# Optimization experiments

Hardware: AMD Instinct MI355X
Metric: run time of the kernel (lower is better)

Reference implementation:

```python
import jax, jax.numpy as jnp
import numpy as np

NUM_EMBEDDINGS = 1024
EMBEDDING_DIM = 256


def setup_inputs() -> dict:
    key = jax.random.key(0)
    k1, k2 = jax.random.split(key)
    input = jax.random.normal(k1, (64, 32, 32, EMBEDDING_DIM), dtype=jnp.float32)
    weight = jax.random.normal(k2, (NUM_EMBEDDINGS, EMBEDDING_DIM), dtype=jnp.float32)
    return {"input": input, "weight": weight}


def reference(input, weight):
    # Nearest-code lookup: argmin_k 0.5*||mu_k||^2 - <z, mu_k>  (scaled by 2 here,
    # matching torch: sqr - 2*cov). weight: [K, D], input: [..., D].
    sqr = jnp.sum(weight * weight, axis=1)                      # [K]
    cov = jnp.einsum('...j,kj->...k', input, weight)            # [..., K]
    indices = jnp.argmin(sqr - 2.0 * cov, axis=-1)              # [...]
    vectors = jnp.take(weight, indices, axis=0)                 # [..., D]
    # Straight-through estimator: values == vectors, grad flows to input.
    values = jax.lax.stop_gradient(vectors - input) + input
    return values, indices, vectors
```

## Files before the change

### kernel.cpp

```cpp
#include <hip/hip_runtime.h>


constexpr int N_TOK = 65536;
constexpr int KC    = 1024;
constexpr int D     = 256;

constexpr size_t IDX_OFF = (size_t)N_TOK * D;
constexpr size_t VEC_OFF = IDX_OFF + N_TOK;
constexpr int    WL_CAP  = 16777216;

#define MARGIN 12.0f

typedef __attribute__((ext_vector_type(8))) short bf16x8;
typedef __attribute__((ext_vector_type(4))) float f32x4;

__device__ inline unsigned short f2bf(float x) {
    unsigned int u = __float_as_uint(x);
    unsigned int r = (u + 0x7FFFu + ((u >> 16) & 1u)) >> 16;
    return (unsigned short)r;
}

__device__ inline unsigned int fkey(float f) {
    unsigned int b = __float_as_uint(f);
    return (b & 0x80000000u) ? ~b : (b | 0x80000000u);
}

__global__ __launch_bounds__(64)
void vq_prep(const float* __restrict__ w, unsigned short* __restrict__ wbf,
             float* __restrict__ sqr, int* __restrict__ cnt) {
    const int code = blockIdx.x;
    const int lane = threadIdx.x;
    float4 v = ((const float4*)w)[(size_t)code * 64 + lane];
    float s = v.x * v.x + v.y * v.y + v.z * v.z + v.w * v.w;
#pragma unroll
    for (int off = 32; off >= 1; off >>= 1) s += __shfl_xor(s, off, 64);
    unsigned short* d = wbf + (size_t)code * D + lane * 4;
    d[0] = f2bf(v.x); d[1] = f2bf(v.y); d[2] = f2bf(v.z); d[3] = f2bf(v.w);
    if (lane == 0) sqr[code] = s;
    if (code == 0 && lane == 0) *cnt = 0;
}

constexpr int CT   = 32;
constexpr int NS   = KC / CT;
constexpr int LCAP = 3072;

struct __align__(16) P1Shared {
    unsigned short sbuf[2][CT * D];
    float sqr[KC];
    int   list[LCAP];
    int   lcnt, gbase;
};

__device__ __forceinline__ void stage32(const unsigned short* __restrict__ wbf,
                                        unsigned short* dstbuf, int s, int tid) {
#pragma unroll
    for (int r = 0; r < 4; ++r) {
        const int dchunk = tid + r * 256;
        const int cc     = dchunk >> 5;
        const int ch     = dchunk & 31;
        const unsigned short* src =
            wbf + (((size_t)(s * CT + cc)) << 8) + ((ch ^ (cc & 7)) << 3);
        unsigned short* dst = dstbuf + (dchunk << 3);
        __builtin_amdgcn_global_load_lds(
            (const __attribute__((address_space(1))) void*)src,
            (__attribute__((address_space(3))) void*)dst, 16, 0, 0);
    }
}

template<bool EMIT>
__device__ __forceinline__ void scan(const unsigned short* __restrict__ wbf,
                                     P1Shared& sh,
                                     const bf16x8 (&a)[2][8],
                                     float (&rmin)[2][4],
                                     int row_base, int tid, int lane, int col, int quad,
                                     int* __restrict__ wl, int* __restrict__ cnt) {
    stage32(wbf, sh.sbuf[0], 0, tid);
    __syncthreads();
    for (int s = 0; s < NS; ++s) {
        if (s + 1 < NS) stage32(wbf, sh.sbuf[(s + 1) & 1], s + 1, tid);
        const unsigned short* sb = sh.sbuf[s & 1];
#pragma unroll
        for (int tt = 0; tt < 2; ++tt) {
            const int ccl = tt * 16 + col;
            const int c0  = s * CT + tt * 16;
            bf16x8 b[8];
#pragma unroll
            for (int kt = 0; kt < 8; ++kt) {
                const int ch = (quad + 4 * kt) ^ (ccl & 7);
                b[kt] = *(const bf16x8*)(sb + ccl * 256 + ch * 8);
            }
            const float sq = sh.sqr[c0 + col];
#pragma unroll
            for (int rt = 0; rt < 2; ++rt) {
                f32x4 acc = {0.f, 0.f, 0.f, 0.f};
#pragma unroll
                for (int kt = 0; kt < 8; ++kt)
                    acc = __builtin_amdgcn_mfma_f32_16x16x32_bf16(a[rt][kt], b[kt], acc, 0, 0, 0);
                if (!EMIT) {
#pragma unroll
                    for (int rg = 0; rg < 4; ++rg)
                        rmin[rt][rg] = fminf(rmin[rt][rg], sq - 2.0f * acc[rg]);
                } else {
#pragma unroll
                    for (int rg = 0; rg < 4; ++rg) {
                        const float sc = sq - 2.0f * acc[rg];
                        const bool flag = (sc <= rmin[rt][rg] + MARGIN);
                        unsigned long long mask = __ballot(flag);
                        if (mask) {
                            const int leader = __builtin_ctzll(mask);
                            const int nact   = __popcll(mask);
                            const int prefix = __popcll(mask & ((1ULL << lane) - 1ULL));
                            int wbase = 0;
                            if (lane == leader) wbase = atomicAdd(&sh.lcnt, nact);
                            wbase = __shfl(wbase, leader, 64);
                            if (flag) {
                                const int row  = row_base + rt * 16 + quad * 4 + rg;
                                const int item = (row << 10) | (c0 + col);
                                const int pos  = wbase + prefix;
                                if (pos < LCAP) {
                                    sh.list[pos] = item;
                                } else {
                                    int g = atomicAdd(cnt, 1);
                                    if (g < WL_CAP) wl[g] = item;
                                }
                            }
                        }
                    }
                }
            }
        }
        __syncthreads();
    }
}

__global__ __launch_bounds__(256)
void vq_pass1(const float* __restrict__ input, const unsigned short* __restrict__ wbf,
              const float* __restrict__ sqr, int* __restrict__ wl,
              int* __restrict__ cnt, unsigned long long* __restrict__ cand) {
    __shared__ P1Shared sh;

    const int tid  = threadIdx.x;
    const int wave = tid >> 6;
    const int lane = tid & 63;
    const int col  = lane & 15;
    const int quad = lane >> 4;
    const int row_base = blockIdx.x * 128 + wave * 32;

    if (tid == 0) sh.lcnt = 0;
    ((float4*)sh.sqr)[tid] = ((const float4*)sqr)[tid];
    if (lane < 32) cand[row_base + lane] = 0xFFFFFFFFFFFFFFFFULL;

    bf16x8 a[2][8];
#pragma unroll
    for (int rt = 0; rt < 2; ++rt) {
        const float* ar = input + (size_t)(row_base + rt * 16 + col) * D;
#pragma unroll
        for (int kt = 0; kt < 8; ++kt) {
            const int k0 = kt * 32 + quad * 8;
            float4 f0 = *(const float4*)(ar + k0);
            float4 f1 = *(const float4*)(ar + k0 + 4);
            bf16x8 v;
            v[0] = (short)f2bf(f0.x); v[1] = (short)f2bf(f0.y);
            v[2] = (short)f2bf(f0.z); v[3] = (short)f2bf(f0.w);
            v[4] = (short)f2bf(f1.x); v[5] = (short)f2bf(f1.y);
            v[6] = (short)f2bf(f1.z); v[7] = (short)f2bf(f1.w);
            a[rt][kt] = v;
        }
    }

    float rmin[2][4];
#pragma unroll
    for (int rt = 0; rt < 2; ++rt)
#pragma unroll
        for (int rg = 0; rg < 4; ++rg) rmin[rt][rg] = 3.4e38f;

    scan<false>(wbf, sh, a, rmin, row_base, tid, lane, col, quad, wl, cnt);

#pragma unroll
    for (int off = 1; off <= 8; off <<= 1)
#pragma unroll
        for (int rt = 0; rt < 2; ++rt)
#pragma unroll
            for (int rg = 0; rg < 4; ++rg)
                rmin[rt][rg] = fminf(rmin[rt][rg], __shfl_xor(rmin[rt][rg], off, 64));

    scan<true>(wbf, sh, a, rmin, row_base, tid, lane, col, quad, wl, cnt);

    __syncthreads();
    const int n = min(sh.lcnt, LCAP);
    if (tid == 0) sh.gbase = atomicAdd(cnt, n);
    __syncthreads();
    const int base = sh.gbase;
    for (int i = tid; i < n; i += 256) wl[base + i] = sh.list[i];
}

__global__ __launch_bounds__(256)
void vq_pass2(const float* __restrict__ input, const float* __restrict__ weight,
              const float* __restrict__ sqr, const int* __restrict__ wl,
              const int* __restrict__ cnt, unsigned long long* __restrict__ cand) {
    const int sw  = threadIdx.x >> 4;
    const int sl  = threadIdx.x & 15;
    const int gsw = blockIdx.x * 16 + sw;
    const int nsw = gridDim.x * 16;
    const int n   = min(*cnt, WL_CAP);
    const float4* in4 = (const float4*)input;
    const float4* w4  = (const float4*)weight;

    for (int e = gsw; e < n; e += nsw) {
        const int ent  = wl[e];
        const int row  = ent >> 10;
        const int code = ent & 1023;
        const float4* zr = in4 + (size_t)row * 64;
        const float4* wr = w4 + (size_t)code * 64;
        float s = 0.f;
#pragma unroll
        for (int j = 0; j < 4; ++j) {
            float4 za = zr[sl + 16 * j];
            float4 wa = wr[sl + 16 * j];
            s = fmaf(za.x, wa.x, s);
            s = fmaf(za.y, wa.y, s);
            s = fmaf(za.z, wa.z, s);
            s = fmaf(za.w, wa.w, s);
        }
#pragma unroll
        for (int off = 1; off <= 8; off <<= 1) s += __shfl_xor(s, off, 16);
        if (sl == 0) {
            const float score = sqr[code] - 2.0f * s;
            unsigned long long key =
                ((unsigned long long)fkey(score) << 32) | (unsigned int)code;
            atomicMin(&cand[row], key);
        }
    }
}

__global__ __launch_bounds__(256)
void vq_pass3(const float* __restrict__ weight,
              const unsigned long long* __restrict__ cand,
              float* __restrict__ out) {
    __shared__ int fin[64];
    const int tid  = threadIdx.x;
    const int row0 = blockIdx.x * 64;
    if (tid < 64) {
        int idx = (int)(unsigned int)(cand[row0 + tid] & 0xFFFFFFFFULL);
        fin[tid] = idx;
        out[IDX_OFF + row0 + tid] = (float)idx;
    }
    __syncthreads();
    const float4* w4 = (const float4*)weight;
    float4* out4 = (float4*)out;
#pragma unroll
    for (int k = 0; k < 16; ++k) {
        int i = tid + k * 256;
        int r = i >> 6, q = i & 63;
        float4 v = w4[(size_t)fin[r] * 64 + q];
        size_t o = (size_t)(row0 + r) * 64 + q;
        out4[o] = v;
        out4[VEC_OFF / 4 + o] = v;
    }
}

extern "C" void kernel_launch(void* const* d_in, const int* in_sizes, int n_in,
                              void* d_out, int out_size, void* d_ws, size_t ws_size,
                              hipStream_t stream) {
    const float* input  = (const float*)d_in[0];
    const float* weight = (const float*)d_in[1];
    float* out = (float*)d_out;

    unsigned short* wbf = (unsigned short*)d_ws;
    float* sqr = (float*)((char*)d_ws + 524288);
    int*   cnt = (int*)((char*)d_ws + 528384);
    unsigned long long* cand = (unsigned long long*)((char*)d_ws + 532480);

    int* wl = (int*)out;

    vq_prep <<<KC, 64, 0, stream>>>(weight, wbf, sqr, cnt);
    vq_pass1<<<N_TOK / 128, 256, 0, stream>>>(input, wbf, sqr, wl, cnt, cand);
    vq_pass2<<<1024, 256, 0, stream>>>(input, weight, sqr, wl, cnt, cand);
    vq_pass3<<<N_TOK / 64, 256, 0, stream>>>(weight, cand, out);
}
```

Baseline: 306.3 us.

## Tile pass1 as 2x2 waves with triple-buffered codebook staging

Pass 1 now arranges its four waves in a 2x2 grid: each wave handles 64 rows and 16 codes per stage, instead of 32 rows over all 32 codes. This halves the LDS B-fragment reads per MFMA. Codebook staging moves to three buffers with two stages in flight, explicit vmcnt waits and a single barrier per stage. The staging source offsets are precomputed so that LDS reads become contiguous, and the per-row minima from the two column waves are merged through shared memory. The A-fragment registers double, and launch bounds ask for two blocks per CU, which adds register pressure and a larger LDS footprint.

```diff
diff --git a/kernel.cpp b/kernel.cpp
--- a/kernel.cpp
+++ b/kernel.cpp
@@ -41,99 +41,99 @@
 }
 
 constexpr int CT   = 32;
-constexpr int NS   = KC / CT;
+constexpr int NSTG = KC / CT;
 constexpr int LCAP = 3072;
 
 struct __align__(16) P1Shared {
-    unsigned short sbuf[2][CT * D];
+    unsigned short sbuf[3][CT * D];
     float sqr[KC];
+    float rminx[2][128];
     int   list[LCAP];
     int   lcnt, gbase;
 };
 
-__device__ __forceinline__ void stage32(const unsigned short* __restrict__ wbf,
-                                        unsigned short* dstbuf, int s, int tid) {
+__device__ __forceinline__ void stage_issue(const char* __restrict__ srcbase,
+                                            unsigned short* __restrict__ dstbuf,
+                                            const int (&soff)[4], int tid) {
 #pragma unroll
     for (int r = 0; r < 4; ++r) {
-        const int dchunk = tid + r * 256;
-        const int cc     = dchunk >> 5;
-        const int ch     = dchunk & 31;
-        const unsigned short* src =
-            wbf + (((size_t)(s * CT + cc)) << 8) + ((ch ^ (cc & 7)) << 3);
-        unsigned short* dst = dstbuf + (dchunk << 3);
         __builtin_amdgcn_global_load_lds(
-            (const __attribute__((address_space(1))) void*)src,
-            (__attribute__((address_space(3))) void*)dst, 16, 0, 0);
+            (const __attribute__((address_space(1))) void*)(srcbase + soff[r]),
+            (__attribute__((address_space(3))) void*)(dstbuf + (tid + r * 256) * 8),
+            16, 0, 0);
     }
 }
 
 template<bool EMIT>
-__device__ __forceinline__ void scan(const unsigned short* __restrict__ wbf,
-                                     P1Shared& sh,
-                                     const bf16x8 (&a)[2][8],
-                                     float (&rmin)[2][4],
-                                     int row_base, int tid, int lane, int col, int quad,
+__device__ __forceinline__ void scan(const char* __restrict__ wbfB, P1Shared& sh,
+                                     const bf16x8 (&a)[4][8], float (&rmin)[4][4],
+                                     int row_base_blk, int wr, int wc,
+                                     int tid, int lane, int col, int quad,
+                                     const int (&soff)[4],
                                      int* __restrict__ wl, int* __restrict__ cnt) {
-    stage32(wbf, sh.sbuf[0], 0, tid);
-    __syncthreads();
-    for (int s = 0; s < NS; ++s) {
-        if (s + 1 < NS) stage32(wbf, sh.sbuf[(s + 1) & 1], s + 1, tid);
-        const unsigned short* sb = sh.sbuf[s & 1];
-#pragma unroll
-        for (int tt = 0; tt < 2; ++tt) {
-            const int ccl = tt * 16 + col;
-            const int c0  = s * CT + tt * 16;
-            bf16x8 b[8];
-#pragma unroll
-            for (int kt = 0; kt < 8; ++kt) {
-                const int ch = (quad + 4 * kt) ^ (ccl & 7);
-                b[kt] = *(const bf16x8*)(sb + ccl * 256 + ch * 8);
-            }
-            const float sq = sh.sqr[c0 + col];
-#pragma unroll
-            for (int rt = 0; rt < 2; ++rt) {
-                f32x4 acc = {0.f, 0.f, 0.f, 0.f};
-#pragma unroll
-                for (int kt = 0; kt < 8; ++kt)
-                    acc = __builtin_amdgcn_mfma_f32_16x16x32_bf16(a[rt][kt], b[kt], acc, 0, 0, 0);
-                if (!EMIT) {
-#pragma unroll
-                    for (int rg = 0; rg < 4; ++rg)
-                        rmin[rt][rg] = fminf(rmin[rt][rg], sq - 2.0f * acc[rg]);
-                } else {
-#pragma unroll
-                    for (int rg = 0; rg < 4; ++rg) {
-                        const float sc = sq - 2.0f * acc[rg];
-                        const bool flag = (sc <= rmin[rt][rg] + MARGIN);
-                        unsigned long long mask = __ballot(flag);
-                        if (mask) {
-                            const int leader = __builtin_ctzll(mask);
-                            const int nact   = __popcll(mask);
-                            const int prefix = __popcll(mask & ((1ULL << lane) - 1ULL));
-                            int wbase = 0;
-                            if (lane == leader) wbase = atomicAdd(&sh.lcnt, nact);
-                            wbase = __shfl(wbase, leader, 64);
-                            if (flag) {
-                                const int row  = row_base + rt * 16 + quad * 4 + rg;
-                                const int item = (row << 10) | (c0 + col);
-                                const int pos  = wbase + prefix;
-                                if (pos < LCAP) {
-                                    sh.list[pos] = item;
-                                } else {
-                                    int g = atomicAdd(cnt, 1);
-                                    if (g < WL_CAP) wl[g] = item;
-                                }
+    stage_issue(wbfB, sh.sbuf[0], soff, tid);
+    stage_issue(wbfB + 16384, sh.sbuf[1], soff, tid);
+
+    for (int s = 0; s < NSTG; ++s) {
+        if (s == NSTG - 1) asm volatile("s_waitcnt vmcnt(0)" ::: "memory");
+        else               asm volatile("s_waitcnt vmcnt(4)" ::: "memory");
+        __builtin_amdgcn_sched_barrier(0);
+        __builtin_amdgcn_s_barrier();
+        __builtin_amdgcn_sched_barrier(0);
+        if (s + 2 < NSTG)
+            stage_issue(wbfB + (s + 2) * 16384, sh.sbuf[(s + 2) % 3], soff, tid);
+
+        const unsigned short* sb =
+            sh.sbuf[s % 3] + wc * 4096 + (quad * 16 + col) * 8;
+        bf16x8 b[8];
+#pragma unroll
+        for (int kt = 0; kt < 8; ++kt)
+            b[kt] = *(const bf16x8*)(sb + kt * 512);
+
+        const int c0 = s * CT + wc * 16;
+        const float sq = sh.sqr[c0 + col];
+#pragma unroll
+        for (int rt = 0; rt < 4; ++rt) {
+            f32x4 acc = {0.f, 0.f, 0.f, 0.f};
+#pragma unroll
+            for (int kt = 0; kt < 8; ++kt)
+                acc = __builtin_amdgcn_mfma_f32_16x16x32_bf16(a[rt][kt], b[kt], acc, 0, 0, 0);
+            if (!EMIT) {
+#pragma unroll
+                for (int rg = 0; rg < 4; ++rg)
+                    rmin[rt][rg] = fminf(rmin[rt][rg], sq - 2.0f * acc[rg]);
+            } else {
+#pragma unroll
+                for (int rg = 0; rg < 4; ++rg) {
+                    const float sc = sq - 2.0f * acc[rg];
+                    const bool flag = (sc <= rmin[rt][rg] + MARGIN);
+                    unsigned long long mask = __ballot(flag);
+                    if (mask) {
+                        const int leader = __builtin_ctzll(mask);
+                        const int nact   = __popcll(mask);
+                        const int prefix = __popcll(mask & ((1ULL << lane) - 1ULL));
+                        int wbase = 0;
+                        if (lane == leader) wbase = atomicAdd(&sh.lcnt, nact);
+                        wbase = __shfl(wbase, leader, 64);
+                        if (flag) {
+                            const int row  = row_base_blk + wr * 64 + rt * 16 + quad * 4 + rg;
+                            const int item = (row << 10) | (c0 + col);
+                            const int pos  = wbase + prefix;
+                            if (pos < LCAP) {
+                                sh.list[pos] = item;
+                            } else {
+                                int g = atomicAdd(cnt, 1);
+                                if (g < WL_CAP) wl[g] = item;
                             }
                         }
                     }
                 }
             }
         }
-        __syncthreads();
-    }
-}
-
-__global__ __launch_bounds__(256)
+    }
+}
+
+__global__ __launch_bounds__(256, 2)
 void vq_pass1(const float* __restrict__ input, const unsigned short* __restrict__ wbf,
               const float* __restrict__ sqr, int* __restrict__ wl,
               int* __restrict__ cnt, unsigned long long* __restrict__ cand) {
@@ -144,16 +144,27 @@
     const int lane = tid & 63;
     const int col  = lane & 15;
     const int quad = lane >> 4;
-    const int row_base = blockIdx.x * 128 + wave * 32;
+    const int wr   = wave >> 1;
+    const int wc   = wave & 1;
+    const int row_base_blk = blockIdx.x * 128;
 
     if (tid == 0) sh.lcnt = 0;
     ((float4*)sh.sqr)[tid] = ((const float4*)sqr)[tid];
-    if (lane < 32) cand[row_base + lane] = 0xFFFFFFFFFFFFFFFFULL;
-
-    bf16x8 a[2][8];
-#pragma unroll
-    for (int rt = 0; rt < 2; ++rt) {
-        const float* ar = input + (size_t)(row_base + rt * 16 + col) * D;
+    if (tid < 128) cand[row_base_blk + tid] = 0xFFFFFFFFFFFFFFFFULL;
+
+    int soff[4];
+#pragma unroll
+    for (int r = 0; r < 4; ++r) {
+        const int sl = tid + r * 256;
+        const int cc = ((sl >> 9) << 4) + (sl & 15);
+        const int ch = (((sl >> 6) & 7) << 2) + ((sl >> 4) & 3);
+        soff[r] = cc * 512 + ch * 16;
+    }
+
+    bf16x8 a[4][8];
+#pragma unroll
+    for (int rt = 0; rt < 4; ++rt) {
+        const float* ar = input + (size_t)(row_base_blk + wr * 64 + rt * 16 + col) * D;
 #pragma unroll
         for (int kt = 0; kt < 8; ++kt) {
             const int k0 = kt * 32 + quad * 8;
@@ -168,23 +179,42 @@
         }
     }
 
-    float rmin[2][4];
-#pragma unroll
-    for (int rt = 0; rt < 2; ++rt)
+    float rmin[4][4];
+#pragma unroll
+    for (int rt = 0; rt < 4; ++rt)
 #pragma unroll
         for (int rg = 0; rg < 4; ++rg) rmin[rt][rg] = 3.4e38f;
 
-    scan<false>(wbf, sh, a, rmin, row_base, tid, lane, col, quad, wl, cnt);
+    __syncthreads();
+
+    scan<false>((const char*)wbf, sh, a, rmin, row_base_blk, wr, wc,
+                tid, lane, col, quad, soff, wl, cnt);
 
 #pragma unroll
     for (int off = 1; off <= 8; off <<= 1)
 #pragma unroll
-        for (int rt = 0; rt < 2; ++rt)
+        for (int rt = 0; rt < 4; ++rt)
 #pragma unroll
             for (int rg = 0; rg < 4; ++rg)
                 rmin[rt][rg] = fminf(rmin[rt][rg], __shfl_xor(rmin[rt][rg], off, 64));
 
-    scan<true>(wbf, sh, a, rmin, row_base, tid, lane, col, quad, wl, cnt);
+    if (col == 0) {
+#pragma unroll
+        for (int rt = 0; rt < 4; ++rt)
+#pragma unroll
+            for (int rg = 0; rg < 4; ++rg)
+                sh.rminx[wc][wr * 64 + rt * 16 + quad * 4 + rg] = rmin[rt][rg];
+    }
+    __syncthreads();
+#pragma unroll
+    for (int rt = 0; rt < 4; ++rt)
+#pragma unroll
+        for (int rg = 0; rg < 4; ++rg)
+            rmin[rt][rg] = fminf(rmin[rt][rg],
+                                 sh.rminx[wc ^ 1][wr * 64 + rt * 16 + quad * 4 + rg]);
+
+    scan<true>((const char*)wbf, sh, a, rmin, row_base_blk, wr, wc,
+               tid, lane, col, quad, soff, wl, cnt);
 
     __syncthreads();
     const int n = min(sh.lcnt, LCAP);
```

Result: slower. 323.0 us (+5.5%).
